# Optimization experiments

Measured on AMD Instinct MI355X. Metric: run time of the kernel, lower is better.

## Reference

```python
import jax, jax.numpy as jnp
import numpy as np

B, H, W, C = 8, 128, 128, 192
WS, SS, HEADS = 8, 4, 6
NW = (H // WS) * (W // WS)
N = WS * WS

def _rel_pos_index(ws):
    coords = np.stack(np.meshgrid(np.arange(ws), np.arange(ws), indexing='ij')).reshape(2, -1)
    rel = (coords[:, :, None] - coords[:, None, :]).transpose(1, 2, 0)
    rel[:, :, 0] += ws - 1
    rel[:, :, 1] += ws - 1
    rel[:, :, 0] *= 2 * ws - 1
    return rel.sum(-1)  # (N, N) int

REL_IDX = jnp.asarray(_rel_pos_index(WS).reshape(-1))

def setup_inputs():
    key = jax.random.key(0)
    ks = jax.random.split(key, 8)
    p = lambda k, shp: jax.random.normal(k, shp, jnp.float32) * 0.02
    # exact Swin shift mask for shift=(SS,SS)
    img = np.zeros((1, H, W, 1), np.float32)
    cnt = 0
    for hs in (slice(0, -WS), slice(-WS, -SS), slice(-SS, None)):
        for vs in (slice(0, -WS), slice(-WS, -SS), slice(-SS, None)):
            img[:, hs, vs, :] = cnt; cnt += 1
    mw = img.reshape(1, H // WS, WS, W // WS, WS, 1).transpose(0, 1, 3, 2, 4, 5).reshape(-1, N)
    diff = mw[:, None, :] - mw[:, :, None]
    mask = np.where(diff != 0, -100.0, 0.0).astype(np.float32)
    return dict(
        x=jax.random.normal(ks[0], (B, H, W, C), jnp.float32),
        mask_matrix=jnp.asarray(mask),
        norm1_g=jnp.ones((C,), jnp.float32), norm1_b=jnp.zeros((C,), jnp.float32),
        qkv_w=p(ks[1], (C, 3 * C)), qkv_b=jnp.zeros((3 * C,), jnp.float32),
        rel_bias_table=p(ks[2], ((2 * WS - 1) * (2 * WS - 1), HEADS)),
        proj_w=p(ks[3], (C, C)), proj_b=jnp.zeros((C,), jnp.float32),
        norm2_g=jnp.ones((C,), jnp.float32), norm2_b=jnp.zeros((C,), jnp.float32),
        fc1_w=p(ks[4], (C, 4 * C)), fc1_b=jnp.zeros((4 * C,), jnp.float32),
        fc2_w=p(ks[5], (4 * C, C)), fc2_b=jnp.zeros((C,), jnp.float32),
    )

def _ln(x, g, b):
    m = x.mean(-1, keepdims=True)
    v = x.var(-1, keepdims=True)
    return (x - m) * jax.lax.rsqrt(v + 1e-5) * g + b

def _window_attn(xw, mask, qkv_w, qkv_b, rel_bias_table, proj_w, proj_b):
    Bw = xw.shape[0]
    hd = C // HEADS
    scale = hd ** -0.5
    # ---- spatial window attention ----
    qkv = (xw @ qkv_w + qkv_b).reshape(Bw, N, 3, HEADS, hd).transpose(2, 0, 3, 1, 4)
    q, k, v = qkv[0], qkv[1], qkv[2]  # (Bw, heads, N, hd)
    attn = jnp.einsum('bhnd,bhmd->bhnm', q, k) * scale
    bias = rel_bias_table[REL_IDX].reshape(N, N, HEADS).transpose(2, 0, 1)
    attn = attn + bias[None]
    attn = attn.reshape(Bw // NW, NW, HEADS, N, N) + mask[None, :, None]
    attn = jax.nn.softmax(attn.reshape(Bw, HEADS, N, N), axis=-1)
    x_spatial = jnp.einsum('bhnm,bhmd->bhnd', attn, v).transpose(0, 2, 1, 3).reshape(Bw, N, C)
    # ---- Fourier-domain attention branch ----
    x2d = xw.reshape(Bw, WS, WS, C)
    xf = jnp.fft.rfftn(x2d, axes=(1, 2), norm='ortho')  # (Bw, WS, WS//2+1, C) complex
    Hf, Wf = xf.shape[1], xf.shape[2]
    Nf = Hf * Wf
    def _qkv(r):  # shared qkv linear applied to real/imag parts (bias in both)
        return (r.reshape(Bw, Nf, C) @ qkv_w + qkv_b).reshape(Bw, Nf, 3, HEADS, hd).transpose(2, 0, 3, 1, 4)
    qr, qi = _qkv(xf.real), _qkv(xf.imag)
    qf = jax.lax.complex(qr[0], qi[0])
    kf = jax.lax.complex(qr[1], qi[1])
    vf = jax.lax.complex(qr[2], qi[2])
    attn_f = jnp.einsum('bhnd,bhmd->bhnm', qf, kf) * scale  # plain transpose, no conj (matches torch)
    attn_mag = jax.nn.softmax(jnp.abs(attn_f), axis=-1)
    xf_res = jnp.einsum('bhnm,bhmd->bhnd', attn_mag.astype(jnp.complex64), vf)
    xf_res = xf_res.transpose(0, 2, 1, 3).reshape(Bw, Hf, Wf, C)
    x_four = jnp.fft.irfftn(xf_res, s=(WS, WS), axes=(1, 2), norm='ortho').reshape(Bw, N, C)
    return (x_spatial + x_four) @ proj_w + proj_b

def reference(x, mask_matrix, norm1_g, norm1_b, qkv_w, qkv_b, rel_bias_table,
              proj_w, proj_b, norm2_g, norm2_b, fc1_w, fc1_b, fc2_w, fc2_b):
    shortcut = x
    xn = _ln(x, norm1_g, norm1_b)
    # shift (H,W divisible by WS so no padding needed)
    xs = jnp.roll(xn, (-SS, -SS), axis=(1, 2))
    # window partition -> (B*nW, N, C)
    xw = xs.reshape(B, H // WS, WS, W // WS, WS, C).transpose(0, 1, 3, 2, 4, 5).reshape(-1, N, C)
    aw = _window_attn(xw, mask_matrix, qkv_w, qkv_b, rel_bias_table, proj_w, proj_b)
    # window reverse + unshift
    xs = aw.reshape(B, H // WS, W // WS, WS, WS, C).transpose(0, 1, 3, 2, 4, 5).reshape(B, H, W, C)
    xo = jnp.roll(xs, (SS, SS), axis=(1, 2))
    x1 = shortcut + xo
    y = _ln(x1, norm2_g, norm2_b)
    y = jax.nn.gelu(y @ fc1_w + fc1_b, approximate=False) @ fc2_w + fc2_b
    return x1 + y
```

## Files before the change

### kernel.cpp

```cpp
#include <hip/hip_runtime.h>
#include <hip/hip_bf16.h>
#include <math.h>

#define SSH 4
#define SCALE 0.17677669529663687f

typedef __bf16 bf16x8 __attribute__((ext_vector_type(8)));
typedef __bf16 bf16x4 __attribute__((ext_vector_type(4)));
typedef unsigned short ushort8 __attribute__((ext_vector_type(8)));
typedef float  f32x4  __attribute__((ext_vector_type(4)));

static __device__ __forceinline__ f32x4 mfma16(bf16x8 a, bf16x8 b, f32x4 c){
    return __builtin_amdgcn_mfma_f32_16x16x32_bf16(a, b, c, 0, 0, 0);
}
#define MFMA16(a,b,c) mfma16((a),(b),(c))

static __device__ __forceinline__ bf16x8 ldfrag(const __bf16* p){
    return *reinterpret_cast<const bf16x8*>(p);
}
static __device__ __forceinline__ f32x4 zero4(){
    f32x4 z; z[0]=0.f; z[1]=0.f; z[2]=0.f; z[3]=0.f; return z;
}
static __device__ __forceinline__ float gelu_fast(float x){
    float u = x*(0.7978845608f + 0.0356774081f*x*x);
    return __fdividef(x, 1.f + __expf(-2.f*u));
}

__global__ __launch_bounds__(256) void k_prep(const float* __restrict__ qkvw,
        const float* __restrict__ projw, const float* __restrict__ fc1w,
        const float* __restrict__ fc2w, __bf16* __restrict__ Wq,
        __bf16* __restrict__ Wp, __bf16* __restrict__ W1, __bf16* __restrict__ W2,
        __bf16* __restrict__ Fre, __bf16* __restrict__ Fim,
        __bf16* __restrict__ Ci,  __bf16* __restrict__ nSi){
    int i = blockIdx.x*256 + threadIdx.x;
    if (i < 110592){ int n = i/192, k = i - n*192; Wq[i] = (__bf16)qkvw[k*576 + n]; }
    if (i < 36864) { int n = i/192, k = i - n*192; Wp[i] = (__bf16)projw[k*192 + n]; }
    if (i < 147456){ int n = i/192, k = i - n*192; W1[i] = (__bf16)fc1w[k*768 + n]; }
    if (i < 147456){ int n = i/768, k = i - n*768; W2[i] = (__bf16)fc2w[k*192 + n]; }
    if (i < 3072){
        int n = i>>6, p = i&63;
        float vr = 0.f, vi = 0.f;
        if (n < 40){
            int u = n/5, v = n - u*5, r = p>>3, c = p&7;
            int k = (u*r + v*c)&7;
            float ang = (float)k * 0.78539816339744831f;
            vr = cosf(ang)*0.125f; vi = -sinf(ang)*0.125f;
        }
        Fre[i] = (__bf16)vr; Fim[i] = (__bf16)vi;
    }
    if (i < 4096){
        int p = i>>6, n = i&63;
        float vc = 0.f, vs = 0.f;
        if (n < 40){
            int u = n/5, v = n - u*5, r = p>>3, c = p&7;
            int k = (u*r + v*c)&7;
            float ang = (float)k * 0.78539816339744831f;
            float wv = (v>=1 && v<=3)? 2.f : 1.f;
            vc = wv*cosf(ang)*0.125f; vs = -wv*sinf(ang)*0.125f;
        }
        Ci[i] = (__bf16)vc; nSi[i] = (__bf16)vs;
    }
}

__global__ __launch_bounds__(256,2) void k_qkv(const float* __restrict__ x,
        const float* __restrict__ n1g, const float* __restrict__ n1b,
        const __bf16* __restrict__ Wqt, const float* __restrict__ qkv_b,
        __bf16* __restrict__ S){
    __shared__ __align__(16) __bf16 xw[64*200];
    __shared__ __align__(16) __bf16 Wt[192*72];
    __shared__ __align__(16) __bf16 Ss[64*200];
    int tid = threadIdx.x;
    int win = blockIdx.x;
    int bb = win>>8, rem = win&255, wh = rem>>4, wwi = rem&15;
    {
        int tok = tid>>2, part = tid&3;
        int r = tok>>3, c = tok&7;
        int sh = (wh*8 + r + SSH)&127, sw = (wwi*8 + c + SSH)&127;
        const float* srcp = x + (((size_t)(bb*128+sh))*128 + sw)*192 + part*48;
        float v[48];
        #pragma unroll
        for (int i=0;i<12;i++){
            float4 t4 = *reinterpret_cast<const float4*>(srcp + i*4);
            v[i*4]=t4.x; v[i*4+1]=t4.y; v[i*4+2]=t4.z; v[i*4+3]=t4.w;
        }
        float s=0.f, ss=0.f;
        #pragma unroll
        for (int i=0;i<48;i++){ s+=v[i]; ss+=v[i]*v[i]; }
        s  += __shfl_xor(s,1);  s  += __shfl_xor(s,2);
        ss += __shfl_xor(ss,1); ss += __shfl_xor(ss,2);
        float mean = s*(1.f/192.f);
        float rstd = rsqrtf(ss*(1.f/192.f) - mean*mean + 1e-5f);
        #pragma unroll
        for (int i8=0;i8<6;i8++){
            bf16x8 pk;
            #pragma unroll
            for (int j=0;j<8;j++){
                int ch = part*48 + i8*8 + j;
                pk[j] = (__bf16)((v[i8*8+j]-mean)*rstd*n1g[ch] + n1b[ch]);
            }
            *reinterpret_cast<bf16x8*>(&xw[tok*200 + part*48 + i8*8]) = pk;
        }
    }
    int lane = tid&63, w = tid>>6, lr = lane&15, lg = lane>>4;
    ushort8 wreg[6];
    auto ldW = [&](int s, ushort8* wr){
        int nc = s/3, kc = s - nc*3;
        #pragma unroll
        for (int i=0;i<6;i++){
            int e = tid + i*256;
            int j = e>>3, k8 = e&7;
            wr[i] = *reinterpret_cast<const ushort8*>(
                reinterpret_cast<const unsigned short*>(Wqt) + (size_t)(nc*192+j)*192 + kc*64 + k8*8);
        }
    };
    auto stW = [&](ushort8* wr){
        #pragma unroll
        for (int i=0;i<6;i++){
            int e = tid + i*256;
            int j = e>>3, k8 = e&7;
            *reinterpret_cast<ushort8*>(reinterpret_cast<unsigned short*>(Wt) + j*72 + k8*8) = wr[i];
        }
    };
    ldW(0, wreg);
    __syncthreads();
    stW(wreg);
    __syncthreads();
    f32x4 acc[4][3];
    #pragma unroll
    for (int m=0;m<4;m++)
        #pragma unroll
        for (int n=0;n<3;n++) acc[m][n] = zero4();
    for (int s=0; s<9; s++){
        int nc = s/3, kc = s - nc*3;
        if (s<8) ldW(s+1, wreg);
        #pragma unroll
        for (int kk=0; kk<2; kk++){
            int ko = kc*64 + kk*32 + lg*8;
            bf16x8 a[4];
            #pragma unroll
            for (int m=0;m<4;m++) a[m] = ldfrag(&xw[(16*m+lr)*200 + ko]);
            int klo = kk*32 + lg*8;
            bf16x8 bfr[3];
            #pragma unroll
            for (int n=0;n<3;n++) bfr[n] = ldfrag(&Wt[(48*w+16*n+lr)*72 + klo]);
            #pragma unroll
            for (int m=0;m<4;m++)
                #pragma unroll
                for (int n=0;n<3;n++) acc[m][n] = MFMA16(a[m], bfr[n], acc[m][n]);
        }
        if (kc==2){
            #pragma unroll
            for (int n=0;n<3;n++){
                int colL = 48*w + 16*n + lr;
                float bias = qkv_b[nc*192 + colL];
                #pragma unroll
                for (int m=0;m<4;m++)
                    #pragma unroll
                    for (int r=0;r<4;r++){
                        Ss[(16*m + 4*lg + r)*200 + colL] = (__bf16)(acc[m][n][r] + bias);
                        acc[m][n][r] = 0.f;
                    }
            }
        }
        __syncthreads();
        if (kc==2){
            #pragma unroll
            for (int i=0;i<6;i++){
                int e = tid + i*256;
                int row = e/24, c8 = e - row*24;
                *reinterpret_cast<bf16x8*>(S + (size_t)(win*64+row)*576 + nc*192 + c8*8) =
                    *reinterpret_cast<const bf16x8*>(&Ss[row*200 + c8*8]);
            }
        }
        if (s<8) stW(wreg);
        __syncthreads();
    }
}

__global__ __launch_bounds__(256,4) void k_spatial(const __bf16* __restrict__ S,
        const float* __restrict__ relt, const float* __restrict__ mask,
        float* __restrict__ Bbuf){
    __shared__ __align__(16) __bf16 P[64*72];
    __shared__ __align__(16) __bf16 Vt[32*72];
    __shared__ float reltL[1350];
    int tid = threadIdx.x;
    int win = blockIdx.x;
    int widx = win & 255;
    int lane = tid&63, w = tid>>6, lr = lane&15, lg = lane>>4;
    for (int e=tid; e<1350; e+=256) reltL[e] = relt[e];
    float mreg[16];
    int bidx[16];
    #pragma unroll
    for (int nt=0; nt<4; nt++)
        #pragma unroll
        for (int r=0;r<4;r++){
            int row = 16*w + 4*lg + r;
            int col = 16*nt + lr;
            mreg[nt*4+r] = mask[((widx*64 + row)<<6) + col];
            int dr = (row>>3)-(col>>3)+7, dc = (row&7)-(col&7)+7;
            bidx[nt*4+r] = (dr*15+dc)*6;
        }
    const size_t sbase = (size_t)win*64*576;
    const __bf16* Sq = S + sbase;
    const __bf16* Sk = S + sbase + 192;
    const __bf16* Sv = S + sbase + 384;
    for (int h=0; h<6; h++){
        __syncthreads();
        {
            int d = tid&31, pg = tid>>5;
            const __bf16* sp = Sv + (size_t)(pg*8)*576 + h*32 + d;
            bf16x4 v0, v1;
            v0[0]=sp[0];    v0[1]=sp[576];  v0[2]=sp[1152]; v0[3]=sp[1728];
            v1[0]=sp[2304]; v1[1]=sp[2880]; v1[2]=sp[3456]; v1[3]=sp[4032];
            *reinterpret_cast<bf16x4*>(&Vt[d*72 + pg*8])   = v0;
            *reinterpret_cast<bf16x4*>(&Vt[d*72 + pg*8+4]) = v1;
        }
        __syncthreads();
        bf16x8 aq = ldfrag(Sq + (size_t)(16*w+lr)*576 + h*32 + lg*8);
        f32x4 acc[4];
        #pragma unroll
        for (int nt=0;nt<4;nt++){
            bf16x8 bk = ldfrag(Sk + (size_t)(16*nt+lr)*576 + h*32 + lg*8);
            acc[nt] = MFMA16(aq, bk, zero4());
        }
        float p[16];
        #pragma unroll
        for (int r=0;r<4;r++){
            float sc[4];
            #pragma unroll
            for (int nt=0;nt<4;nt++)
                sc[nt] = acc[nt][r]*SCALE + reltL[bidx[nt*4+r] + h] + mreg[nt*4+r];
            float mx = fmaxf(fmaxf(sc[0],sc[1]),fmaxf(sc[2],sc[3]));
            mx = fmaxf(mx, __shfl_xor(mx,1));
            mx = fmaxf(mx, __shfl_xor(mx,2));
            mx = fmaxf(mx, __shfl_xor(mx,4));
            mx = fmaxf(mx, __shfl_xor(mx,8));
            float sum = 0.f;
            #pragma unroll
            for (int nt=0;nt<4;nt++){ sc[nt] = __expf(sc[nt]-mx); sum += sc[nt]; }
            sum += __shfl_xor(sum,1);
            sum += __shfl_xor(sum,2);
            sum += __shfl_xor(sum,4);
            sum += __shfl_xor(sum,8);
            float inv = 1.f/sum;
            #pragma unroll
            for (int nt=0;nt<4;nt++) p[r*4+nt] = sc[nt]*inv;
        }
        #pragma unroll
        for (int r=0;r<4;r++)
            #pragma unroll
            for (int nt=0;nt<4;nt++)
                P[(16*w + 4*lg + r)*72 + 16*nt + lr] = (__bf16)p[r*4+nt];
        #pragma unroll
        for (int dt=0; dt<2; dt++){
            f32x4 o = zero4();
            #pragma unroll
            for (int ks=0; ks<2; ks++)
                o = MFMA16(ldfrag(&P[(16*w+lr)*72 + ks*32 + lg*8]),
                           ldfrag(&Vt[(16*dt+lr)*72 + ks*32 + lg*8]), o);
            #pragma unroll
            for (int r=0;r<4;r++){
                int row = 16*w + 4*lg + r;
                Bbuf[((size_t)win*64 + row)*192 + h*32 + 16*dt + lr] = o[r];
            }
        }
    }
}

__global__ __launch_bounds__(256,3) void k_fattn(const __bf16* __restrict__ S,
        const float* __restrict__ qkv_b,
        const __bf16* __restrict__ Fre_g, const __bf16* __restrict__ Fim_g,
        const __bf16* __restrict__ Ci_g,  const __bf16* __restrict__ nSi_g,
        float* __restrict__ Bbuf){
    __shared__ __align__(16) unsigned char arena[51968];
    __bf16* Gq_r = (__bf16*)(arena);
    __bf16* Gqin = (__bf16*)(arena + 3840);
    __bf16* Gk_r = (__bf16*)(arena + 7680);
    __bf16* Gk_i = (__bf16*)(arena + 11520);
    __bf16* Rt_r = (__bf16*)(arena);
    __bf16* Rt_i = (__bf16*)(arena + 5632);
    __bf16* Gv_r = (__bf16*)(arena + 15360);
    __bf16* Gv_i = (__bf16*)(arena + 20992);
    __bf16* St3  = (__bf16*)(arena + 26624);
    float*  Smat = (float*) (arena + 26624);
    __bf16* P    = (__bf16*)(arena + 43520);
    int tid = threadIdx.x;
    int win = blockIdx.x / 6, h = blockIdx.x - win*6;
    int lane = tid&63, w = tid>>6, lr = lane&15, lg = lane>>4;
    bf16x4 z4; z4[0]=z4[1]=z4[2]=z4[3]=(__bf16)0.f;
    const size_t sbase = (size_t)win*64*576 + h*32;
    {
        int t2 = tid & 127;
        __bf16* A = (tid<128)? Gv_r : Gv_i;
        int row = t2>>2, c4 = (t2&3)*4;
        *reinterpret_cast<bf16x4*>(A + row*88 + 48 + c4) = z4;
    }
    {
        int d = tid&31, pg = tid>>5;
        #pragma unroll
        for (int m=0;m<3;m++){
            const __bf16* sp = S + sbase + (size_t)m*192 + (size_t)pg*8*576 + d;
            bf16x4 v0, v1;
            v0[0]=sp[0];      v0[1]=sp[576];    v0[2]=sp[1152];   v0[3]=sp[1728];
            v1[0]=sp[2304];   v1[1]=sp[2880];   v1[2]=sp[3456];   v1[3]=sp[4032];
            *reinterpret_cast<bf16x4*>(&St3[m*2816 + d*88 + pg*8])     = v0;
            *reinterpret_cast<bf16x4*>(&St3[m*2816 + d*88 + pg*8 + 4]) = v1;
        }
    }
    __syncthreads();
    for (int j=w; j<36; j+=4){
        int m = j/12, jj = j - m*12;
        int term = jj/6, r2 = jj - term*6;
        const __bf16* Stm = &St3[m*2816];
        if (m<2){
            int mt = r2>>1, nt = r2&1;
            const __bf16* Ag = (term? Fim_g : Fre_g) + (16*mt+lr)*64 + lg*8;
            f32x4 acc = zero4();
            acc = MFMA16(*reinterpret_cast<const bf16x8*>(Ag),
                         ldfrag(&Stm[(16*nt+lr)*88 + lg*8]), acc);
            acc = MFMA16(*reinterpret_cast<const bf16x8*>(Ag+32),
                         ldfrag(&Stm[(16*nt+lr)*88 + 32 + lg*8]), acc);
            int d = 16*nt + lr;
            float b = qkv_b[m*192 + h*32 + d];
            __bf16* dst = (m==0)? (term? Gqin : Gq_r) : (term? Gk_i : Gk_r);
            #pragma unroll
            for (int r=0;r<4;r++){
                int n = 16*mt + 4*lg + r;
                float val = acc[r] + ((term==0) ? ((n==0)? -7.f*b : b) : b);
                if (m==0 && term==1) val = -val;
                dst[n*40 + d] = (__bf16)val;
            }
        } else {
            int mt = r2/3, nt = r2 - mt*3;
            const __bf16* Bg = (term? Fim_g : Fre_g) + (16*nt+lr)*64 + lg*8;
            f32x4 acc = zero4();
            acc = MFMA16(ldfrag(&Stm[(16*mt+lr)*88 + lg*8]),
                         *reinterpret_cast<const bf16x8*>(Bg), acc);
            acc = MFMA16(ldfrag(&Stm[(16*mt+lr)*88 + 32 + lg*8]),
                         *reinterpret_cast<const bf16x8*>(Bg+32), acc);
            int n = 16*nt + lr;
            __bf16* dst = term? Gv_i : Gv_r;
            #pragma unroll
            for (int r=0;r<4;r++){
                int d = 16*mt + 4*lg + r;
                float b = qkv_b[2*192 + h*32 + d];
                float val = acc[r] + ((term==0) ? ((n==0)? -7.f*b : b) : b);
                dst[d*88 + n] = (__bf16)val;
            }
        }
    }
    __syncthreads();
    for (int j=w; j<9; j+=4){
        int mt = j/3, nt = j - mt*3;
        bf16x8 qr = ldfrag(&Gq_r[(16*mt+lr)*40 + lg*8]);
        bf16x8 qi = ldfrag(&Gqin[(16*mt+lr)*40 + lg*8]);
        bf16x8 kr = ldfrag(&Gk_r[(16*nt+lr)*40 + lg*8]);
        bf16x8 ki = ldfrag(&Gk_i[(16*nt+lr)*40 + lg*8]);
        f32x4 sre = MFMA16(qi, ki, zero4());
        sre = MFMA16(qr, kr, sre);
        f32x4 t1 = MFMA16(qr, ki, zero4());
        f32x4 t2 = MFMA16(qi, kr, zero4());
        #pragma unroll
        for (int r=0;r<4;r++){
            float sim = t1[r] - t2[r];
            Smat[(16*mt + 4*lg + r)*52 + 16*nt + lr] =
                SCALE * sqrtf(sre[r]*sre[r] + sim*sim);
        }
    }
    __syncthreads();
    if (tid < 160){
        int row = tid>>2, part = tid&3, e0 = part*10;
        float mx = -1e30f;
        #pragma unroll
        for (int j=0;j<10;j++) mx = fmaxf(mx, Smat[row*52 + e0 + j]);
        mx = fmaxf(mx, __shfl_xor(mx,1));
        mx = fmaxf(mx, __shfl_xor(mx,2));
        float ex[10]; float sum=0.f;
        #pragma unroll
        for (int j=0;j<10;j++){ ex[j] = __expf(Smat[row*52+e0+j]-mx); sum += ex[j]; }
        sum += __shfl_xor(sum,1);
        sum += __shfl_xor(sum,2);
        float inv = 1.f/sum;
        #pragma unroll
        for (int j=0;j<10;j++) Smat[row*52+e0+j] = ex[j]*inv;
    }
    __syncthreads();
    for (int e=tid; e<3072; e+=256){
        int row = e>>6, col = e&63;
        float v = (row<40 && col<40)? Smat[row*52+col] : 0.f;
        P[row*88+col] = (__bf16)v;
    }
    {
        int t2 = tid & 127;
        __bf16* A = (tid<128)? Rt_r : Rt_i;
        int row = t2>>2, c4 = (t2&3)*4;
        *reinterpret_cast<bf16x4*>(A + row*88 + 48 + c4) = z4;
    }
    __syncthreads();
    for (int j=w; j<12; j+=4){
        int term = j/6, r2 = j - term*6;
        int dt = r2/3, nt = r2 - dt*3;
        const __bf16* Gv = term? Gv_i : Gv_r;
        f32x4 acc = zero4();
        #pragma unroll
        for (int ks=0; ks<2; ks++)
            acc = MFMA16(ldfrag(&Gv[(16*dt+lr)*88 + ks*32 + lg*8]),
                         ldfrag(&P [(16*nt+lr)*88 + ks*32 + lg*8]), acc);
        __bf16* dst = term? Rt_i : Rt_r;
        #pragma unroll
        for (int r=0;r<4;r++)
            dst[(16*dt + 4*lg + r)*88 + 16*nt + lr] = (__bf16)acc[r];
    }
    __syncthreads();
    for (int j=w; j<8; j+=4){
        int dt = j>>2, pt = j&3;
        f32x4 acc = zero4();
        #pragma unroll
        for (int ks=0; ks<2; ks++)
            acc = MFMA16(*reinterpret_cast<const bf16x8*>(nSi_g + (16*pt+lr)*64 + ks*32 + lg*8),
                         ldfrag(&Rt_i[(16*dt+lr)*88 + ks*32 + lg*8]), acc);
        #pragma unroll
        for (int ks=0; ks<2; ks++)
            acc = MFMA16(*reinterpret_cast<const bf16x8*>(Ci_g + (16*pt+lr)*64 + ks*32 + lg*8),
                         ldfrag(&Rt_r[(16*dt+lr)*88 + ks*32 + lg*8]), acc);
        #pragma unroll
        for (int r=0;r<4;r++){
            int p = 16*pt + 4*lg + r, d = 16*dt + lr;
            size_t idx = ((size_t)win*64 + p)*192 + h*32 + d;
            Bbuf[idx] += acc[r];
        }
    }
}

__global__ __launch_bounds__(256,4) void k_proj(const float* __restrict__ Bbuf,
        const float* __restrict__ x, const __bf16* __restrict__ Wpt,
        const float* __restrict__ proj_b, float* __restrict__ X1){
    __shared__ __align__(16) __bf16 xt[64*200];
    int tid = threadIdx.x;
    int win = blockIdx.x;
    {
        int tok = tid>>2, part = tid&3;
        const float* srcp = Bbuf + ((size_t)win*64 + tok)*192 + part*48;
        #pragma unroll
        for (int i8=0;i8<6;i8++){
            float4 a4 = *reinterpret_cast<const float4*>(srcp + i8*8);
            float4 b4 = *reinterpret_cast<const float4*>(srcp + i8*8 + 4);
            bf16x8 pk;
            pk[0]=(__bf16)a4.x; pk[1]=(__bf16)a4.y; pk[2]=(__bf16)a4.z; pk[3]=(__bf16)a4.w;
            pk[4]=(__bf16)b4.x; pk[5]=(__bf16)b4.y; pk[6]=(__bf16)b4.z; pk[7]=(__bf16)b4.w;
            *reinterpret_cast<bf16x8*>(&xt[tok*200 + part*48 + i8*8]) = pk;
        }
    }
    __syncthreads();
    int lane = tid&63, w = tid>>6, lr = lane&15, lg = lane>>4;
    f32x4 acc[4][3];
    #pragma unroll
    for (int m=0;m<4;m++)
        #pragma unroll
        for (int n=0;n<3;n++) acc[m][n] = zero4();
    #pragma unroll
    for (int kc=0; kc<6; kc++){
        int ko = kc*32 + lg*8;
        bf16x8 a[4];
        #pragma unroll
        for (int m=0;m<4;m++) a[m] = ldfrag(&xt[(16*m+lr)*200 + ko]);
        bf16x8 bfr[3];
        #pragma unroll
        for (int n=0;n<3;n++)
            bfr[n] = ldfrag(Wpt + (size_t)(48*w + 16*n + lr)*192 + ko);
        #pragma unroll
        for (int m=0;m<4;m++)
            #pragma unroll
            for (int n=0;n<3;n++) acc[m][n] = MFMA16(a[m], bfr[n], acc[m][n]);
    }
    int bb = win>>8, rem = win&255, wh = rem>>4, wwi = rem&15;
    #pragma unroll
    for (int m=0;m<4;m++)
        #pragma unroll
        for (int r=0;r<4;r++){
            int t = 16*m + 4*lg + r;
            int p = wh*8 + (t>>3), q = wwi*8 + (t&7);
            int hh = (p+SSH)&127, w2 = (q+SSH)&127;
            size_t pixb = (((size_t)bb*128 + hh)*128 + w2)*192;
            #pragma unroll
            for (int n=0;n<3;n++){
                int col = 48*w + 16*n + lr;
                X1[pixb + col] = acc[m][n][r] + proj_b[col] + x[pixb + col];
            }
        }
}

__global__ __launch_bounds__(256,3) void k_mlp(const float* __restrict__ X1,
        const float* __restrict__ g2, const float* __restrict__ b2v,
        const __bf16* __restrict__ W1t, const float* __restrict__ fc1b,
        const __bf16* __restrict__ W2t, const float* __restrict__ fc2b,
        float* __restrict__ out){
    __shared__ __align__(16) __bf16 xln[64*200];
    __shared__ __align__(16) __bf16 hbuf[64*200];
    int tid = threadIdx.x;
    size_t base = (size_t)blockIdx.x*64;
    {
        int tok = tid>>2, part = tid&3;
        const float* srcp = X1 + (base + tok)*192 + part*48;
        float v[48];
        #pragma unroll
        for (int i=0;i<12;i++){
            float4 t4 = *reinterpret_cast<const float4*>(srcp + i*4);
            v[i*4]=t4.x; v[i*4+1]=t4.y; v[i*4+2]=t4.z; v[i*4+3]=t4.w;
        }
        float s=0.f, ss=0.f;
        #pragma unroll
        for (int i=0;i<48;i++){ s+=v[i]; ss+=v[i]*v[i]; }
        s  += __shfl_xor(s,1);  s  += __shfl_xor(s,2);
        ss += __shfl_xor(ss,1); ss += __shfl_xor(ss,2);
        float mean = s*(1.f/192.f);
        float rstd = rsqrtf(ss*(1.f/192.f) - mean*mean + 1e-5f);
        #pragma unroll
        for (int i8=0;i8<6;i8++){
            bf16x8 pk;
            #pragma unroll
            for (int j=0;j<8;j++){
                int ch = part*48 + i8*8 + j;
                pk[j] = (__bf16)((v[i8*8+j]-mean)*rstd*g2[ch] + b2v[ch]);
            }
            *reinterpret_cast<bf16x8*>(&xln[tok*200 + part*48 + i8*8]) = pk;
        }
    }
    __syncthreads();
    int lane = tid&63, w = tid>>6, lr = lane&15, lg = lane>>4;
    f32x4 acc2[4][3];
    #pragma unroll
    for (int m=0;m<4;m++)
        #pragma unroll
        for (int n=0;n<3;n++) acc2[m][n] = zero4();
    for (int hc=0; hc<4; hc++){
        f32x4 acc1[4][3];
        #pragma unroll
        for (int m=0;m<4;m++)
            #pragma unroll
            for (int n=0;n<3;n++) acc1[m][n] = zero4();
        #pragma unroll
        for (int kc=0; kc<6; kc++){
            int ko = kc*32 + lg*8;
            bf16x8 a[4];
            #pragma unroll
            for (int m=0;m<4;m++) a[m] = ldfrag(&xln[(16*m+lr)*200 + ko]);
            bf16x8 bfr[3];
            #pragma unroll
            for (int n=0;n<3;n++)
                bfr[n] = ldfrag(W1t + (size_t)(hc*192 + 48*w + 16*n + lr)*192 + ko);
            #pragma unroll
            for (int m=0;m<4;m++)
                #pragma unroll
                for (int n=0;n<3;n++) acc1[m][n] = MFMA16(a[m], bfr[n], acc1[m][n]);
        }
        #pragma unroll
        for (int n=0;n<3;n++){
            int jcol = 48*w + 16*n + lr;
            float b1 = fc1b[hc*192 + jcol];
            #pragma unroll
            for (int m=0;m<4;m++)
                #pragma unroll
                for (int r=0;r<4;r++){
                    float xv = acc1[m][n][r] + b1;
                    hbuf[(16*m + 4*lg + r)*200 + jcol] = (__bf16)gelu_fast(xv);
                }
        }
        __syncthreads();
        #pragma unroll
        for (int kc=0; kc<6; kc++){
            int ko = kc*32 + lg*8;
            bf16x8 a[4];
            #pragma unroll
            for (int m=0;m<4;m++) a[m] = ldfrag(&hbuf[(16*m+lr)*200 + ko]);
            bf16x8 bfr[3];
            #pragma unroll
            for (int n=0;n<3;n++)
                bfr[n] = ldfrag(W2t + (size_t)(48*w + 16*n + lr)*768 + hc*192 + ko);
            #pragma unroll
            for (int m=0;m<4;m++)
                #pragma unroll
                for (int n=0;n<3;n++) acc2[m][n] = MFMA16(a[m], bfr[n], acc2[m][n]);
        }
        __syncthreads();
    }
    #pragma unroll
    for (int n=0;n<3;n++){
        int col = 48*w + 16*n + lr;
        float b2 = fc2b[col];
        #pragma unroll
        for (int m=0;m<4;m++)
            #pragma unroll
            for (int r=0;r<4;r++){
                size_t t = base + 16*m + 4*lg + r;
                out[t*192 + col] = acc2[m][n][r] + b2 + X1[t*192 + col];
            }
    }
}

extern "C" void kernel_launch(void* const* d_in, const int* in_sizes, int n_in,
                              void* d_out, int out_size, void* d_ws, size_t ws_size,
                              hipStream_t stream) {
    const float* x     = (const float*)d_in[0];
    const float* mask  = (const float*)d_in[1];
    const float* n1g   = (const float*)d_in[2];
    const float* n1b   = (const float*)d_in[3];
    const float* qkvw  = (const float*)d_in[4];
    const float* qkvb  = (const float*)d_in[5];
    const float* relt  = (const float*)d_in[6];
    const float* projw = (const float*)d_in[7];
    const float* projb = (const float*)d_in[8];
    const float* n2g   = (const float*)d_in[9];
    const float* n2b   = (const float*)d_in[10];
    const float* fc1w  = (const float*)d_in[11];
    const float* fc1b  = (const float*)d_in[12];
    const float* fc2w  = (const float*)d_in[13];
    const float* fc2b  = (const float*)d_in[14];
    float* out = (float*)d_out;

    char* wsb = (char*)d_ws;
    __bf16* Sb  = (__bf16*)wsb;
    float*  X1  = (float*)(wsb + 150994944);
    __bf16* Wqt = (__bf16*)(wsb + 251658240);
    __bf16* Wpt = (__bf16*)(wsb + 251879424);
    __bf16* W1t = (__bf16*)(wsb + 251953152);
    __bf16* W2t = (__bf16*)(wsb + 252248064);
    __bf16* Fre = (__bf16*)(wsb + 252542976);
    __bf16* Fim = (__bf16*)(wsb + 252549120);
    __bf16* Ci  = (__bf16*)(wsb + 252555264);
    __bf16* nSi = (__bf16*)(wsb + 252563456);

    k_prep   <<<576,   256, 0, stream>>>(qkvw, projw, fc1w, fc2w, Wqt, Wpt, W1t, W2t,
                                         Fre, Fim, Ci, nSi);
    k_qkv    <<<2048,  256, 0, stream>>>(x, n1g, n1b, Wqt, qkvb, Sb);
    k_spatial<<<2048,  256, 0, stream>>>(Sb, relt, mask, out);
    k_fattn  <<<12288, 256, 0, stream>>>(Sb, qkvb, Fre, Fim, Ci, nSi, out);
    k_proj   <<<2048,  256, 0, stream>>>(out, x, Wpt, projb, X1);
    k_mlp    <<<2048,  256, 0, stream>>>(X1, n2g, n2b, W1t, fc1b, W2t, fc2b, out);
}
```

Baseline: 599.9 us.

## Fuse projection and MLP into one per-window kernel, dropping X1 round trip

Merges k_proj and k_mlp into a single k_ffn kernel per window. The proj+residual result is kept in LDS and registers as bf16 rather than written to an fp32 X1 buffer and read back. This removes one full activation write and two reads from global memory plus a kernel launch. In exchange the launch bound drops to two blocks per CU, and the residual x1 is now stored in bf16, which loses precision in both the LayerNorm input and the final residual add.

```diff
diff --git a/kernel.cpp b/kernel.cpp
--- a/kernel.cpp
+++ b/kernel.cpp
@@ -432,10 +432,14 @@
     }
 }
 
-__global__ __launch_bounds__(256,4) void k_proj(const float* __restrict__ Bbuf,
+__global__ __launch_bounds__(256,2) void k_ffn(const float* __restrict__ Bbuf,
         const float* __restrict__ x, const __bf16* __restrict__ Wpt,
-        const float* __restrict__ proj_b, float* __restrict__ X1){
+        const float* __restrict__ proj_b, const float* __restrict__ g2,
+        const float* __restrict__ b2v, const __bf16* __restrict__ W1t,
+        const float* __restrict__ fc1b, const __bf16* __restrict__ W2t,
+        const float* __restrict__ fc2b, float* __restrict__ out){
     __shared__ __align__(16) __bf16 xt[64*200];
+    __shared__ __align__(16) __bf16 yb[64*200];
     int tid = threadIdx.x;
     int win = blockIdx.x;
     {
@@ -474,6 +478,7 @@
             for (int n=0;n<3;n++) acc[m][n] = MFMA16(a[m], bfr[n], acc[m][n]);
     }
     int bb = win>>8, rem = win&255, wh = rem>>4, wwi = rem&15;
+    bf16x4 yreg[4][3];
     #pragma unroll
     for (int m=0;m<4;m++)
         #pragma unroll
@@ -485,28 +490,21 @@
             #pragma unroll
             for (int n=0;n<3;n++){
                 int col = 48*w + 16*n + lr;
-                X1[pixb + col] = acc[m][n][r] + proj_b[col] + x[pixb + col];
-            }
-        }
-}
-
-__global__ __launch_bounds__(256,3) void k_mlp(const float* __restrict__ X1,
-        const float* __restrict__ g2, const float* __restrict__ b2v,
-        const __bf16* __restrict__ W1t, const float* __restrict__ fc1b,
-        const __bf16* __restrict__ W2t, const float* __restrict__ fc2b,
-        float* __restrict__ out){
-    __shared__ __align__(16) __bf16 xln[64*200];
-    __shared__ __align__(16) __bf16 hbuf[64*200];
-    int tid = threadIdx.x;
-    size_t base = (size_t)blockIdx.x*64;
+                float yv = acc[m][n][r] + proj_b[col] + x[pixb + col];
+                __bf16 yh = (__bf16)yv;
+                yreg[m][n][r] = yh;
+                yb[t*200 + col] = yh;
+            }
+        }
+    __syncthreads();
     {
         int tok = tid>>2, part = tid&3;
-        const float* srcp = X1 + (base + tok)*192 + part*48;
         float v[48];
         #pragma unroll
-        for (int i=0;i<12;i++){
-            float4 t4 = *reinterpret_cast<const float4*>(srcp + i*4);
-            v[i*4]=t4.x; v[i*4+1]=t4.y; v[i*4+2]=t4.z; v[i*4+3]=t4.w;
+        for (int i8=0;i8<6;i8++){
+            bf16x8 pk = *reinterpret_cast<const bf16x8*>(&yb[tok*200 + part*48 + i8*8]);
+            #pragma unroll
+            for (int j=0;j<8;j++) v[i8*8+j] = (float)pk[j];
         }
         float s=0.f, ss=0.f;
         #pragma unroll
@@ -523,11 +521,10 @@
                 int ch = part*48 + i8*8 + j;
                 pk[j] = (__bf16)((v[i8*8+j]-mean)*rstd*g2[ch] + b2v[ch]);
             }
-            *reinterpret_cast<bf16x8*>(&xln[tok*200 + part*48 + i8*8]) = pk;
-        }
-    }
-    __syncthreads();
-    int lane = tid&63, w = tid>>6, lr = lane&15, lg = lane>>4;
+            *reinterpret_cast<bf16x8*>(&yb[tok*200 + part*48 + i8*8]) = pk;
+        }
+    }
+    __syncthreads();
     f32x4 acc2[4][3];
     #pragma unroll
     for (int m=0;m<4;m++)
@@ -544,7 +541,7 @@
             int ko = kc*32 + lg*8;
             bf16x8 a[4];
             #pragma unroll
-            for (int m=0;m<4;m++) a[m] = ldfrag(&xln[(16*m+lr)*200 + ko]);
+            for (int m=0;m<4;m++) a[m] = ldfrag(&yb[(16*m+lr)*200 + ko]);
             bf16x8 bfr[3];
             #pragma unroll
             for (int n=0;n<3;n++)
@@ -563,7 +560,7 @@
                 #pragma unroll
                 for (int r=0;r<4;r++){
                     float xv = acc1[m][n][r] + b1;
-                    hbuf[(16*m + 4*lg + r)*200 + jcol] = (__bf16)gelu_fast(xv);
+                    xt[(16*m + 4*lg + r)*200 + jcol] = (__bf16)gelu_fast(xv);
                 }
         }
         __syncthreads();
@@ -572,7 +569,7 @@
             int ko = kc*32 + lg*8;
             bf16x8 a[4];
             #pragma unroll
-            for (int m=0;m<4;m++) a[m] = ldfrag(&hbuf[(16*m+lr)*200 + ko]);
+            for (int m=0;m<4;m++) a[m] = ldfrag(&xt[(16*m+lr)*200 + ko]);
             bf16x8 bfr[3];
             #pragma unroll
             for (int n=0;n<3;n++)
@@ -585,17 +582,19 @@
         __syncthreads();
     }
     #pragma unroll
-    for (int n=0;n<3;n++){
-        int col = 48*w + 16*n + lr;
-        float b2 = fc2b[col];
-        #pragma unroll
-        for (int m=0;m<4;m++)
-            #pragma unroll
-            for (int r=0;r<4;r++){
-                size_t t = base + 16*m + 4*lg + r;
-                out[t*192 + col] = acc2[m][n][r] + b2 + X1[t*192 + col];
-            }
-    }
+    for (int m=0;m<4;m++)
+        #pragma unroll
+        for (int r=0;r<4;r++){
+            int t = 16*m + 4*lg + r;
+            int p = wh*8 + (t>>3), q = wwi*8 + (t&7);
+            int hh = (p+SSH)&127, w2 = (q+SSH)&127;
+            size_t pixb = (((size_t)bb*128 + hh)*128 + w2)*192;
+            #pragma unroll
+            for (int n=0;n<3;n++){
+                int col = 48*w + 16*n + lr;
+                out[pixb + col] = acc2[m][n][r] + fc2b[col] + (float)yreg[m][n][r];
+            }
+        }
 }
 
 extern "C" void kernel_launch(void* const* d_in, const int* in_sizes, int n_in,
@@ -619,8 +618,8 @@
     float* out = (float*)d_out;
 
     char* wsb = (char*)d_ws;
-    __bf16* Sb  = (__bf16*)wsb;
-    float*  X1  = (float*)(wsb + 150994944);
+    __bf16* Sb   = (__bf16*)wsb;
+    float*  Bbuf = (float*)(wsb + 150994944);
     __bf16* Wqt = (__bf16*)(wsb + 251658240);
     __bf16* Wpt = (__bf16*)(wsb + 251879424);
     __bf16* W1t = (__bf16*)(wsb + 251953152);
@@ -633,8 +632,8 @@
     k_prep   <<<576,   256, 0, stream>>>(qkvw, projw, fc1w, fc2w, Wqt, Wpt, W1t, W2t,
                                          Fre, Fim, Ci, nSi);
     k_qkv    <<<2048,  256, 0, stream>>>(x, n1g, n1b, Wqt, qkvb, Sb);
-    k_spatial<<<2048,  256, 0, stream>>>(Sb, relt, mask, out);
-    k_fattn  <<<12288, 256, 0, stream>>>(Sb, qkvb, Fre, Fim, Ci, nSi, out);
-    k_proj   <<<2048,  256, 0, stream>>>(out, x, Wpt, projb, X1);
-    k_mlp    <<<2048,  256, 0, stream>>>(X1, n2g, n2b, W1t, fc1b, W2t, fc2b, out);
-}
+    k_spatial<<<2048,  256, 0, stream>>>(Sb, relt, mask, Bbuf);
+    k_fattn  <<<12288, 256, 0, stream>>>(Sb, qkvb, Fre, Fim, Ci, nSi, Bbuf);
+    k_ffn    <<<2048,  256, 0, stream>>>(Bbuf, x, Wpt, projb, n2g, n2b,
+                                         W1t, fc1b, W2t, fc2b, out);
+}
```

Result: no change. 595.4 us (-0.8%).
